# Kernel optimization log

Hardware: AMD Instinct MI355X
Metric: run time of the kernel (lower is better)

The kernel has to match this reference:

```python
import jax, jax.numpy as jnp
import numpy as np

B, N, M = 2, 16200, 128
DIM, QK_DIM, HEADS, GS = 256, 256, 8, 128


def setup_inputs() -> dict:
    key = jax.random.key(0)
    ks = jax.random.split(key, 10)
    sorted_x = jax.random.normal(ks[0], (B, N, DIM), dtype=jnp.float32)
    prototypes = jax.random.normal(ks[1], (B, M, DIM), dtype=jnp.float32)
    # idx_last must be a per-batch permutation of 0..N-1 (scatter-back to original order)
    idx_last = jnp.argsort(jax.random.uniform(ks[2], (B, N)), axis=-1).astype(jnp.int32)[..., None]
    s = 0.02
    Wq = jax.random.normal(ks[3], (DIM, QK_DIM), dtype=jnp.float32) * s
    Wk = jax.random.normal(ks[4], (DIM, QK_DIM), dtype=jnp.float32) * s
    Wv = jax.random.normal(ks[5], (DIM, DIM), dtype=jnp.float32) * s
    Wpk = jax.random.normal(ks[6], (DIM, QK_DIM), dtype=jnp.float32) * s
    Wpv = jax.random.normal(ks[7], (DIM, DIM), dtype=jnp.float32) * s
    Wproj = jax.random.normal(ks[8], (DIM, DIM), dtype=jnp.float32) * s
    return {"sorted_x": sorted_x, "idx_last": idx_last, "prototypes": prototypes,
            "Wq": Wq, "Wk": Wk, "Wv": Wv, "Wpk": Wpk, "Wpv": Wpv, "Wproj": Wproj}


def _iasa(sorted_x, idx_last, prototypes, Wq, Wk, Wv, Wpk, Wpv, Wproj):
    b, n, dim = sorted_x.shape
    h = HEADS
    gs = min(n, GS)
    ng = (n + gs - 1) // gs
    pad_n = ng * gs - n
    dq = Wq.shape[1] // h   # qk head dim
    dv = Wv.shape[1] // h   # v head dim
    scale = 1.0 / jnp.sqrt(jnp.asarray(dq, sorted_x.dtype))

    q = sorted_x @ Wq
    k = sorted_x @ Wk
    v = sorted_x @ Wv

    # pad q with flipped tail (pad_n tokens) -> [b, ng*gs, qk]
    q_pad = jnp.concatenate([q, q[:, n - pad_n:n][:, ::-1]], axis=1)
    qh = q_pad.reshape(b, ng, gs, h, dq).transpose(0, 1, 3, 2, 4)  # b ng h gs d

    def windows(t, c):
        # pad with flipped last (pad_n + gs) tokens -> length (ng+1)*gs, then
        # overlapping windows of 2*gs with stride gs (== torch unfold)
        t_pad = jnp.concatenate([t, t[:, n - pad_n - gs:n][:, ::-1]], axis=1)
        tr = t_pad.reshape(b, ng + 1, gs, c)
        win = jnp.concatenate([tr[:, :-1], tr[:, 1:]], axis=2)  # b ng 2gs c
        return win.reshape(b, ng, 2 * gs, h, c // h).transpose(0, 1, 3, 2, 4)  # b ng h 2gs d

    kw = windows(k, Wk.shape[1])
    vw = windows(v, Wv.shape[1])

    # local overlapping-window attention
    a1 = jax.nn.softmax(jnp.einsum('bghqd,bghkd->bghqk', qh, kw) * scale, axis=-1)
    o1 = jnp.einsum('bghqk,bghkd->bghqd', a1, vw)

    # global prototype cross-attention
    kg = (prototypes @ Wpk).reshape(b, -1, h, dq).transpose(0, 2, 1, 3)  # b h m d
    vg = (prototypes @ Wpv).reshape(b, -1, h, dv).transpose(0, 2, 1, 3)
    a2 = jax.nn.softmax(jnp.einsum('bghqd,bhmd->bghqm', qh, kg) * scale, axis=-1)
    o2 = jnp.einsum('bghqm,bhmd->bghqd', a2, vg)

    out = (o1 + o2).transpose(0, 1, 3, 2, 4).reshape(b, ng * gs, h * dv)[:, :n]

    # scatter back to original order: result[b, idx[b,i], c] = out[b, i, c]
    idx = jnp.broadcast_to(idx_last, out.shape)
    b_idx = jnp.arange(b)[:, None, None]
    c_idx = jnp.arange(out.shape[-1])[None, None, :]
    out = out.at[b_idx, idx, c_idx].set(out)
    return out @ Wproj


def reference(sorted_x, idx_last, prototypes, Wq, Wk, Wv, Wpk, Wpv, Wproj):
    return _iasa(sorted_x, idx_last, prototypes, Wq, Wk, Wv, Wpk, Wpv, Wproj)
```

## Files before the change

kernel.cpp:

```cpp
#include <hip/hip_runtime.h>
#include <hip/hip_bf16.h>


typedef unsigned short u16;
typedef unsigned int   u32;
typedef __attribute__((ext_vector_type(8))) u16   u16x8;
typedef __attribute__((ext_vector_type(4))) u16   u16x4;
typedef __attribute__((ext_vector_type(8))) short bf16x8;
typedef __attribute__((ext_vector_type(4))) float f32x4;

#define NB   2
#define NN   16200
#define MM   128
#define NH   8
#define NGRP 127
#define APAD 72

static __device__ __forceinline__ u16 f2bf(float f) {
  u32 u = __float_as_uint(f);
  return (u16)((u + 0x7FFFu + ((u >> 16) & 1u)) >> 16);
}

static __device__ __forceinline__ u16 f2bfn(float f) {
  __hip_bfloat16 h = __float2bfloat16(f);
  u16 r;
  __builtin_memcpy(&r, &h, 2);
  return r;
}

static __device__ __forceinline__ f32x4 mfma16(bf16x8 a, bf16x8 b, f32x4 c) {
  return __builtin_amdgcn_mfma_f32_16x16x32_bf16(a, b, c, 0, 0, 0);
}

__global__ void prep_wt(const float* __restrict__ w0, const float* __restrict__ w1,
                        const float* __restrict__ w2, const float* __restrict__ w3,
                        const float* __restrict__ w4, const float* __restrict__ w5,
                        u16* __restrict__ wt) {
  int m = blockIdx.y;
  const float* W = m == 0 ? w0 : m == 1 ? w1 : m == 2 ? w2 : m == 3 ? w3 : m == 4 ? w4 : w5;
  int t = blockIdx.x * 256 + threadIdx.x;
  int o = t >> 8, i = t & 255;
  wt[((size_t)(m * 256 + o) << 8) + i] = f2bf(W[(i << 8) + o]);
}

template <bool AF32, bool CF32>
__global__ __launch_bounds__(256) void gemm_bt(
    const void* __restrict__ Av, int numRows,
    const u16* __restrict__ Bt,
    void* __restrict__ Cv, int ldc,
    const int* __restrict__ idx)
{
  __shared__ __attribute__((aligned(16))) u16 sA[128 * APAD];
  __shared__ __attribute__((aligned(16))) u16 sB[128 * APAD];
  int rowBase = blockIdx.x << 7;
  int colBase = blockIdx.y << 7;
  int tid = threadIdx.x;
  int lane = tid & 63, w = tid >> 6;
  int wr = (w >> 1) << 6, wc = (w & 1) << 6;
  int lr = lane & 15, lg = lane >> 4;

  f32x4 acc[4][4];
#pragma unroll
  for (int i = 0; i < 4; ++i)
#pragma unroll
    for (int j = 0; j < 4; ++j) acc[i][j] = (f32x4)0.0f;

  for (int kt = 0; kt < 4; ++kt) {
#pragma unroll
    for (int i = 0; i < 4; ++i) {
      int e = tid + (i << 8);
      int r = e >> 3;
      int cc = (e & 7) << 3;
      int gr = rowBase + r;
      gr = gr < numRows ? gr : 0;
      if constexpr (AF32) {
        const float* A = (const float*)Av;
        f32x4 a0 = *(const f32x4*)(A + ((size_t)gr << 8) + (kt << 6) + cc);
        f32x4 a1 = *(const f32x4*)(A + ((size_t)gr << 8) + (kt << 6) + cc + 4);
        u16x8 val;
#pragma unroll
        for (int j = 0; j < 4; ++j) { val[j] = f2bf(a0[j]); val[4 + j] = f2bf(a1[j]); }
        *(u16x8*)(sA + r * APAD + cc) = val;
      } else {
        const u16* A = (const u16*)Av;
        *(u16x8*)(sA + r * APAD + cc) =
            *(const u16x8*)(A + ((size_t)gr << 8) + (kt << 6) + cc);
      }
      *(u16x8*)(sB + r * APAD + cc) =
          *(const u16x8*)(Bt + ((size_t)(colBase + r) << 8) + (kt << 6) + cc);
    }
    __syncthreads();
#pragma unroll
    for (int kk = 0; kk < 2; ++kk) {
      bf16x8 af[4], bfv[4];
#pragma unroll
      for (int m = 0; m < 4; ++m)
        af[m] = *(const bf16x8*)(sA + (wr + (m << 4) + lr) * APAD + (kk << 5) + (lg << 3));
#pragma unroll
      for (int n = 0; n < 4; ++n)
        bfv[n] = *(const bf16x8*)(sB + (wc + (n << 4) + lr) * APAD + (kk << 5) + (lg << 3));
#pragma unroll
      for (int m = 0; m < 4; ++m)
#pragma unroll
        for (int n = 0; n < 4; ++n) acc[m][n] = mfma16(af[m], bfv[n], acc[m][n]);
    }
    __syncthreads();
  }

#pragma unroll
  for (int m = 0; m < 4; ++m) {
    int row0 = rowBase + wr + (m << 4) + (lg << 2);
#pragma unroll
    for (int r = 0; r < 4; ++r) {
      int rr = row0 + r;
      if (rr >= numRows) continue;
      size_t orow = rr;
      if (idx) {
        int b = rr / NN;
        orow = (size_t)b * NN + idx[rr];
      }
#pragma unroll
      for (int n = 0; n < 4; ++n) {
        int col = colBase + wc + (n << 4) + lr;
        if constexpr (CF32) {
          ((float*)Cv)[orow * ldc + col] = acc[m][n][r];
        } else {
          ((u16*)Cv)[orow * ldc + col] = f2bf(acc[m][n][r]);
        }
      }
    }
  }
}

__global__ __launch_bounds__(256) void attn_kernel(
    const u16* __restrict__ qkv,
    const u16* __restrict__ kgvg,
    u16* __restrict__ outa)
{
  __shared__ __attribute__((aligned(16))) u16 sKV[256 * 40];
  __shared__ __attribute__((aligned(16))) u16 sP[4][16 * 264];

  int bid = blockIdx.x;
  int qh = bid & 1;
  int rest = bid >> 1;
  int g = rest % NGRP;
  int h = (rest / NGRP) & 7;
  int b = rest / (NGRP * NH);

  int tid = threadIdx.x, lane = tid & 63, w = tid >> 6;
  int lr = lane & 15, lg = lane >> 4;

  const size_t bOff = (size_t)b * NN * 768;
  const int hoff = h << 5;
  const int kbase = g << 7;

  u16x8 vreg[4];
  int vr_[4], vc_[4];
#pragma unroll
  for (int i = 0; i < 4; ++i) {
    int e = tid + (i << 8);
    int r = e >> 2, c = (e & 3) << 3;
    int kp = kbase + r;
    int tok = kp < NN ? kp : 2 * NN - 1 - kp;
    *(u16x8*)(sKV + r * 40 + c) =
        *(const u16x8*)(qkv + bOff + (size_t)tok * 768 + 256 + hoff + c);
    vreg[i] = *(const u16x8*)(qkv + bOff + (size_t)tok * 768 + 512 + hoff + c);
    vr_[i] = r; vc_[i] = c;
  }
  __syncthreads();

  const float scale = 0.17677669529663687f;
  int qrow = (qh << 6) + (w << 4) + lr;
  int qtok = kbase + qrow;
  qtok = qtok < NN ? qtok : 2 * NN - 1 - qtok;
  bf16x8 qf = *(const bf16x8*)(qkv + bOff + (size_t)qtok * 768 + hoff + (lg << 3));

  f32x4 z = (f32x4)0.0f;
  f32x4 s[16];
#pragma unroll
  for (int kt = 0; kt < 16; ++kt) {
    bf16x8 kf = *(const bf16x8*)(sKV + ((kt << 4) + lr) * 40 + (lg << 3));
    s[kt] = mfma16(kf, qf, z);
  }
  float m0 = -1e30f, m1 = -1e30f, m2 = -1e30f, m3 = -1e30f;
#pragma unroll
  for (int kt = 0; kt < 16; ++kt) {
    m0 = fmaxf(m0, s[kt][0]); m1 = fmaxf(m1, s[kt][1]);
    m2 = fmaxf(m2, s[kt][2]); m3 = fmaxf(m3, s[kt][3]);
  }
  float mx = fmaxf(fmaxf(m0, m1), fmaxf(m2, m3));
  mx = fmaxf(mx, __shfl_xor(mx, 16, 64));
  mx = fmaxf(mx, __shfl_xor(mx, 32, 64));
  float u0 = 0.f, u1 = 0.f, u2 = 0.f, u3 = 0.f;
#pragma unroll
  for (int kt = 0; kt < 16; ++kt) {
    float p0 = __expf((s[kt][0] - mx) * scale);
    float p1 = __expf((s[kt][1] - mx) * scale);
    float p2 = __expf((s[kt][2] - mx) * scale);
    float p3 = __expf((s[kt][3] - mx) * scale);
    s[kt][0] = p0; s[kt][1] = p1; s[kt][2] = p2; s[kt][3] = p3;
    u0 += p0; u1 += p1; u2 += p2; u3 += p3;
  }
  float sum = (u0 + u1) + (u2 + u3);
  sum += __shfl_xor(sum, 16, 64);
  sum += __shfl_xor(sum, 32, 64);
  float inv = 1.0f / sum;
#pragma unroll
  for (int kt = 0; kt < 16; ++kt) {
    u16x4 pk;
#pragma unroll
    for (int r = 0; r < 4; ++r) pk[r] = f2bfn(s[kt][r] * inv);
    *(u16x4*)(&sP[w][lr * 264 + (kt << 4) + (lg << 2)]) = pk;
  }
  __syncthreads();

#pragma unroll
  for (int i = 0; i < 4; ++i) {
    int r = vr_[i], c = vc_[i];
#pragma unroll
    for (int u = 0; u < 8; ++u) {
      int dv = c + u;
      sKV[dv * 264 + (r ^ ((((dv >> 3) & 3)) << 3))] = vreg[i][u];
    }
  }
  __syncthreads();

  const int sw0 = ((lr >> 3) & 3) << 3;
  const int sw1 = (((16 + lr) >> 3) & 3) << 3;

  f32x4 o0 = z, o1 = z;
#pragma unroll
  for (int kb = 0; kb < 8; ++kb) {
    int k0 = (kb << 5) + (lg << 3);
    bf16x8 pf = *(const bf16x8*)(&sP[w][lr * 264 + k0]);
    bf16x8 v0 = *(const bf16x8*)(sKV + lr * 264 + (k0 ^ sw0));
    bf16x8 v1 = *(const bf16x8*)(sKV + (16 + lr) * 264 + (k0 ^ sw1));
    o0 = mfma16(v0, pf, o0);
    o1 = mfma16(v1, pf, o1);
  }

  f32x4 sg[8];
#pragma unroll
  for (int kt = 0; kt < 8; ++kt) {
    bf16x8 kf = *(const bf16x8*)(kgvg + ((size_t)(b * MM + (kt << 4) + lr) << 9) + hoff + (lg << 3));
    sg[kt] = mfma16(kf, qf, z);
  }
  bf16x8 vg0[4], vg1[4];
#pragma unroll
  for (int kb = 0; kb < 4; ++kb) {
#pragma unroll
    for (int j = 0; j < 8; ++j) {
      size_t row = ((size_t)(b * MM + (kb << 5) + (lg << 3) + j) << 9) + 256 + hoff;
      vg0[kb][j] = (short)kgvg[row + lr];
      vg1[kb][j] = (short)kgvg[row + 16 + lr];
    }
  }
  float n0 = -1e30f, n1 = -1e30f, n2 = -1e30f, n3 = -1e30f;
#pragma unroll
  for (int kt = 0; kt < 8; ++kt) {
    n0 = fmaxf(n0, sg[kt][0]); n1 = fmaxf(n1, sg[kt][1]);
    n2 = fmaxf(n2, sg[kt][2]); n3 = fmaxf(n3, sg[kt][3]);
  }
  float mx2 = fmaxf(fmaxf(n0, n1), fmaxf(n2, n3));
  mx2 = fmaxf(mx2, __shfl_xor(mx2, 16, 64));
  mx2 = fmaxf(mx2, __shfl_xor(mx2, 32, 64));
  float t0 = 0.f, t1 = 0.f, t2 = 0.f, t3 = 0.f;
#pragma unroll
  for (int kt = 0; kt < 8; ++kt) {
    float p0 = __expf((sg[kt][0] - mx2) * scale);
    float p1 = __expf((sg[kt][1] - mx2) * scale);
    float p2 = __expf((sg[kt][2] - mx2) * scale);
    float p3 = __expf((sg[kt][3] - mx2) * scale);
    sg[kt][0] = p0; sg[kt][1] = p1; sg[kt][2] = p2; sg[kt][3] = p3;
    t0 += p0; t1 += p1; t2 += p2; t3 += p3;
  }
  float sum2 = (t0 + t1) + (t2 + t3);
  sum2 += __shfl_xor(sum2, 16, 64);
  sum2 += __shfl_xor(sum2, 32, 64);
  float inv2 = 1.0f / sum2;
#pragma unroll
  for (int kt = 0; kt < 8; ++kt) {
    u16x4 pk;
#pragma unroll
    for (int r = 0; r < 4; ++r) pk[r] = f2bfn(sg[kt][r] * inv2);
    *(u16x4*)(&sP[w][lr * 264 + (kt << 4) + (lg << 2)]) = pk;
  }
#pragma unroll
  for (int kb = 0; kb < 4; ++kb) {
    int k0 = (kb << 5) + (lg << 3);
    bf16x8 pf = *(const bf16x8*)(&sP[w][lr * 264 + k0]);
    o0 = mfma16(vg0[kb], pf, o0);
    o1 = mfma16(vg1[kb], pf, o1);
  }

  int token = kbase + (qh << 6) + (w << 4) + lr;
  if (token < NN) {
    size_t base = ((size_t)b * NN + token) * 256 + hoff;
    u16x4 w0v, w1v;
#pragma unroll
    for (int r = 0; r < 4; ++r) {
      w0v[r] = f2bfn(o0[r]);
      w1v[r] = f2bfn(o1[r]);
    }
    *(u16x4*)(outa + base + (lg << 2)) = w0v;
    *(u16x4*)(outa + base + 16 + (lg << 2)) = w1v;
  }
}

extern "C" void kernel_launch(void* const* d_in, const int* in_sizes, int n_in,
                              void* d_out, int out_size, void* d_ws, size_t ws_size,
                              hipStream_t stream) {
  const float* x     = (const float*)d_in[0];
  const int*   idx   = (const int*)d_in[1];
  const float* proto = (const float*)d_in[2];
  const float* Wq    = (const float*)d_in[3];
  const float* Wk    = (const float*)d_in[4];
  const float* Wv    = (const float*)d_in[5];
  const float* Wpk   = (const float*)d_in[6];
  const float* Wpv   = (const float*)d_in[7];
  const float* Wproj = (const float*)d_in[8];

  u16* wt   = (u16*)d_ws;
  u16* qkv  = wt + (size_t)1536 * 256;
  u16* kgvg = qkv + (size_t)32400 * 768;
  u16* attn = kgvg + (size_t)256 * 512;

  prep_wt<<<dim3(256, 6), 256, 0, stream>>>(Wq, Wk, Wv, Wpk, Wpv, Wproj, wt);
  gemm_bt<true, false><<<dim3(254, 6), 256, 0, stream>>>(x, NB * NN, wt, qkv, 768, nullptr);
  gemm_bt<true, false><<<dim3(2, 4), 256, 0, stream>>>(proto, NB * MM, wt + (size_t)768 * 256,
                                                       kgvg, 512, nullptr);
  attn_kernel<<<dim3(NB * NH * NGRP * 2), 256, 0, stream>>>(qkv, kgvg, attn);
  gemm_bt<false, true><<<dim3(254, 2), 256, 0, stream>>>(attn, NB * NN, wt + (size_t)1280 * 256,
                                                         d_out, 256, idx);
}
```

Measured before the change: 225.9 us.

## Write V transposed per head from GEMM epilogue and drop LDS staging in attention

The V projection is split into its own GEMM whose epilogue writes V in a head-major, token-contiguous transposed layout. A small kernel then builds the flipped tail padding and a transposed prototype-V. The attention kernel now reads K and V fragments straight from global memory instead of staging them through shared memory with a transpose and extra barriers. This removes the in-kernel LDS transpose and two syncthreads, but the transposed epilogue writes are scattered 2-byte stores and the GEMM for x is now issued as two launches.

```diff
diff --git a/kernel.cpp b/kernel.cpp
--- a/kernel.cpp
+++ b/kernel.cpp
@@ -43,7 +43,7 @@
   wt[((size_t)(m * 256 + o) << 8) + i] = f2bf(W[(i << 8) + o]);
 }
 
-template <bool AF32, bool CF32>
+template <bool AF32, int CMODE>
 __global__ __launch_bounds__(256) void gemm_bt(
     const void* __restrict__ Av, int numRows,
     const u16* __restrict__ Bt,
@@ -114,30 +114,55 @@
     for (int r = 0; r < 4; ++r) {
       int rr = row0 + r;
       if (rr >= numRows) continue;
-      size_t orow = rr;
-      if (idx) {
-        int b = rr / NN;
-        orow = (size_t)b * NN + idx[rr];
-      }
 #pragma unroll
       for (int n = 0; n < 4; ++n) {
         int col = colBase + wc + (n << 4) + lr;
-        if constexpr (CF32) {
+        if constexpr (CMODE == 0) {
+          ((u16*)Cv)[(size_t)rr * ldc + col] = f2bf(acc[m][n][r]);
+        } else if constexpr (CMODE == 1) {
+          int b = rr >= NN;
+          size_t orow = idx ? ((size_t)b * NN + idx[rr]) : (size_t)rr;
           ((float*)Cv)[orow * ldc + col] = acc[m][n][r];
         } else {
-          ((u16*)Cv)[orow * ldc + col] = f2bf(acc[m][n][r]);
+          int b = rr >= NN;
+          int token = rr - (b ? NN : 0);
+          int hh = col >> 5, dv = col & 31;
+          ((u16*)Cv)[(((size_t)((b << 3) + hh) * 32 + dv) << 14) + token] =
+              f2bf(acc[m][n][r]);
         }
       }
     }
   }
 }
 
+__global__ void vgt_pad(const u16* __restrict__ kgvg, u16* __restrict__ vT,
+                        u16* __restrict__ vgT) {
+  int t = blockIdx.x * 256 + threadIdx.x;
+  if (t < 65536) {
+    int bh = t >> 12;
+    int dv = (t >> 7) & 31;
+    int m  = t & 127;
+    int b = bh >> 3, h = bh & 7;
+    vgT[t] = kgvg[((size_t)(b * MM + m) << 9) + 256 + h * 32 + dv];
+  }
+  int t2 = t - 65536;
+  if (t2 >= 0 && t2 < 94208) {
+    int bh = t2 / 5888;
+    int rem = t2 - bh * 5888;
+    int dv = rem / 184;
+    int j = rem - dv * 184;
+    size_t row = ((size_t)(bh * 32 + dv)) << 14;
+    vT[row + NN + j] = vT[row + NN - 1 - j];
+  }
+}
+
 __global__ __launch_bounds__(256) void attn_kernel(
-    const u16* __restrict__ qkv,
+    const u16* __restrict__ qk,
     const u16* __restrict__ kgvg,
+    const u16* __restrict__ vT,
+    const u16* __restrict__ vgT,
     u16* __restrict__ outa)
 {
-  __shared__ __attribute__((aligned(16))) u16 sKV[256 * 40];
   __shared__ __attribute__((aligned(16))) u16 sP[4][16 * 264];
 
   int bid = blockIdx.x;
@@ -150,36 +175,23 @@
   int tid = threadIdx.x, lane = tid & 63, w = tid >> 6;
   int lr = lane & 15, lg = lane >> 4;
 
-  const size_t bOff = (size_t)b * NN * 768;
+  const u16* qkb = qk + (size_t)b * NN * 512;
   const int hoff = h << 5;
   const int kbase = g << 7;
-
-  u16x8 vreg[4];
-  int vr_[4], vc_[4];
-#pragma unroll
-  for (int i = 0; i < 4; ++i) {
-    int e = tid + (i << 8);
-    int r = e >> 2, c = (e & 3) << 3;
-    int kp = kbase + r;
-    int tok = kp < NN ? kp : 2 * NN - 1 - kp;
-    *(u16x8*)(sKV + r * 40 + c) =
-        *(const u16x8*)(qkv + bOff + (size_t)tok * 768 + 256 + hoff + c);
-    vreg[i] = *(const u16x8*)(qkv + bOff + (size_t)tok * 768 + 512 + hoff + c);
-    vr_[i] = r; vc_[i] = c;
-  }
-  __syncthreads();
 
   const float scale = 0.17677669529663687f;
   int qrow = (qh << 6) + (w << 4) + lr;
   int qtok = kbase + qrow;
   qtok = qtok < NN ? qtok : 2 * NN - 1 - qtok;
-  bf16x8 qf = *(const bf16x8*)(qkv + bOff + (size_t)qtok * 768 + hoff + (lg << 3));
+  bf16x8 qf = *(const bf16x8*)(qkb + (size_t)qtok * 512 + hoff + (lg << 3));
 
   f32x4 z = (f32x4)0.0f;
   f32x4 s[16];
 #pragma unroll
   for (int kt = 0; kt < 16; ++kt) {
-    bf16x8 kf = *(const bf16x8*)(sKV + ((kt << 4) + lr) * 40 + (lg << 3));
+    int kp = kbase + (kt << 4) + lr;
+    int tok = kp < NN ? kp : 2 * NN - 1 - kp;
+    bf16x8 kf = *(const bf16x8*)(qkb + (size_t)tok * 512 + 256 + hoff + (lg << 3));
     s[kt] = mfma16(kf, qf, z);
   }
   float m0 = -1e30f, m1 = -1e30f, m2 = -1e30f, m3 = -1e30f;
@@ -212,29 +224,15 @@
     for (int r = 0; r < 4; ++r) pk[r] = f2bfn(s[kt][r] * inv);
     *(u16x4*)(&sP[w][lr * 264 + (kt << 4) + (lg << 2)]) = pk;
   }
-  __syncthreads();
-
-#pragma unroll
-  for (int i = 0; i < 4; ++i) {
-    int r = vr_[i], c = vc_[i];
-#pragma unroll
-    for (int u = 0; u < 8; ++u) {
-      int dv = c + u;
-      sKV[dv * 264 + (r ^ ((((dv >> 3) & 3)) << 3))] = vreg[i][u];
-    }
-  }
-  __syncthreads();
-
-  const int sw0 = ((lr >> 3) & 3) << 3;
-  const int sw1 = (((16 + lr) >> 3) & 3) << 3;
-
+
+  const u16* vtb = vT + (((size_t)((b << 3) + h) * 32) << 14);
   f32x4 o0 = z, o1 = z;
 #pragma unroll
   for (int kb = 0; kb < 8; ++kb) {
     int k0 = (kb << 5) + (lg << 3);
     bf16x8 pf = *(const bf16x8*)(&sP[w][lr * 264 + k0]);
-    bf16x8 v0 = *(const bf16x8*)(sKV + lr * 264 + (k0 ^ sw0));
-    bf16x8 v1 = *(const bf16x8*)(sKV + (16 + lr) * 264 + (k0 ^ sw1));
+    bf16x8 v0 = *(const bf16x8*)(vtb + ((size_t)lr << 14) + kbase + k0);
+    bf16x8 v1 = *(const bf16x8*)(vtb + ((size_t)(16 + lr) << 14) + kbase + k0);
     o0 = mfma16(v0, pf, o0);
     o1 = mfma16(v1, pf, o1);
   }
@@ -244,16 +242,6 @@
   for (int kt = 0; kt < 8; ++kt) {
     bf16x8 kf = *(const bf16x8*)(kgvg + ((size_t)(b * MM + (kt << 4) + lr) << 9) + hoff + (lg << 3));
     sg[kt] = mfma16(kf, qf, z);
-  }
-  bf16x8 vg0[4], vg1[4];
-#pragma unroll
-  for (int kb = 0; kb < 4; ++kb) {
-#pragma unroll
-    for (int j = 0; j < 8; ++j) {
-      size_t row = ((size_t)(b * MM + (kb << 5) + (lg << 3) + j) << 9) + 256 + hoff;
-      vg0[kb][j] = (short)kgvg[row + lr];
-      vg1[kb][j] = (short)kgvg[row + 16 + lr];
-    }
   }
   float n0 = -1e30f, n1 = -1e30f, n2 = -1e30f, n3 = -1e30f;
 #pragma unroll
@@ -285,12 +273,15 @@
     for (int r = 0; r < 4; ++r) pk[r] = f2bfn(sg[kt][r] * inv2);
     *(u16x4*)(&sP[w][lr * 264 + (kt << 4) + (lg << 2)]) = pk;
   }
+  const u16* vgtb = vgT + (size_t)((b << 3) + h) * 32 * 128;
 #pragma unroll
   for (int kb = 0; kb < 4; ++kb) {
     int k0 = (kb << 5) + (lg << 3);
     bf16x8 pf = *(const bf16x8*)(&sP[w][lr * 264 + k0]);
-    o0 = mfma16(vg0[kb], pf, o0);
-    o1 = mfma16(vg1[kb], pf, o1);
+    bf16x8 v0 = *(const bf16x8*)(vgtb + lr * 128 + k0);
+    bf16x8 v1 = *(const bf16x8*)(vgtb + (16 + lr) * 128 + k0);
+    o0 = mfma16(v0, pf, o0);
+    o1 = mfma16(v1, pf, o1);
   }
 
   int token = kbase + (qh << 6) + (w << 4) + lr;
@@ -321,15 +312,20 @@
   const float* Wproj = (const float*)d_in[8];
 
   u16* wt   = (u16*)d_ws;
-  u16* qkv  = wt + (size_t)1536 * 256;
-  u16* kgvg = qkv + (size_t)32400 * 768;
-  u16* attn = kgvg + (size_t)256 * 512;
+  u16* qk   = wt + (size_t)1536 * 256;
+  u16* kgvg = qk + (size_t)32400 * 512;
+  u16* vgT  = kgvg + (size_t)256 * 512;
+  u16* vT   = vgT + (size_t)16 * 32 * 128;
+  u16* attn = vT + ((size_t)16 * 32 << 14);
 
   prep_wt<<<dim3(256, 6), 256, 0, stream>>>(Wq, Wk, Wv, Wpk, Wpv, Wproj, wt);
-  gemm_bt<true, false><<<dim3(254, 6), 256, 0, stream>>>(x, NB * NN, wt, qkv, 768, nullptr);
-  gemm_bt<true, false><<<dim3(2, 4), 256, 0, stream>>>(proto, NB * MM, wt + (size_t)768 * 256,
-                                                       kgvg, 512, nullptr);
-  attn_kernel<<<dim3(NB * NH * NGRP * 2), 256, 0, stream>>>(qkv, kgvg, attn);
-  gemm_bt<false, true><<<dim3(254, 2), 256, 0, stream>>>(attn, NB * NN, wt + (size_t)1280 * 256,
-                                                         d_out, 256, idx);
-}
+  gemm_bt<true, 0><<<dim3(254, 4), 256, 0, stream>>>(x, NB * NN, wt, qk, 512, nullptr);
+  gemm_bt<true, 2><<<dim3(254, 2), 256, 0, stream>>>(x, NB * NN, wt + (size_t)512 * 256,
+                                                     vT, 0, nullptr);
+  gemm_bt<true, 0><<<dim3(2, 4), 256, 0, stream>>>(proto, NB * MM, wt + (size_t)768 * 256,
+                                                   kgvg, 512, nullptr);
+  vgt_pad<<<dim3((65536 + 94208 + 255) / 256), 256, 0, stream>>>(kgvg, vT, vgT);
+  attn_kernel<<<dim3(NB * NH * NGRP * 2), 256, 0, stream>>>(qk, kgvg, vT, vgT, attn);
+  gemm_bt<false, 1><<<dim3(254, 2), 256, 0, stream>>>(attn, NB * NN, wt + (size_t)1280 * 256,
+                                                      d_out, 256, idx);
+}
```

Result: slower. 270.4 us (+19.7%).
